# Kernel tuning notes

Measured on AMD Instinct MI355X. Metric: run time of the kernel, lower is better.

The kernel has to match this reference:

```python
import jax, jax.numpy as jnp
import numpy as np

EPS = 1e-5

def conv2d(x, w, pad):
    # x: [B,C,H,W], w: [O,I,kh,kw]
    return jax.lax.conv_general_dilated(x, w, window_strides=(1, 1),
                                        padding=[(pad, pad), (pad, pad)],
                                        dimension_numbers=('NCHW', 'OIHW', 'NCHW'))

def bn(x, g, b, m, v):
    # inference-mode BatchNorm2d
    scale = g / jnp.sqrt(v + EPS)
    return x * scale[None, :, None, None] + (b - m * scale)[None, :, None, None]

def setup_inputs() -> dict:
    key = jax.random.key(0)
    ks = jax.random.split(key, 12)
    B, C, H, W = 4, 256, 300, 300
    HC, NC, NREG = 64, 3, 8
    inp = {
        'bev_features': jax.random.normal(ks[0], (B, C, H, W), jnp.float32),
        'w_shared': jax.random.normal(ks[1], (HC, C, 3, 3), jnp.float32) * 0.02,
        'g_shared': jax.random.uniform(ks[2], (HC,), jnp.float32, 0.5, 1.5),
        'b_shared': jnp.zeros((HC,), jnp.float32),
        'm_shared': jnp.zeros((HC,), jnp.float32),
        'v_shared': jnp.ones((HC,), jnp.float32),
        'w_hm1': jax.random.normal(ks[3], (HC, HC, 3, 3), jnp.float32) * 0.05,
        'g_hm1': jax.random.uniform(ks[4], (HC,), jnp.float32, 0.5, 1.5),
        'b_hm1': jnp.zeros((HC,), jnp.float32),
        'm_hm1': jnp.zeros((HC,), jnp.float32),
        'v_hm1': jnp.ones((HC,), jnp.float32),
        'w_hm2': jax.random.normal(ks[5], (NC, HC, 1, 1), jnp.float32) * 0.05,
        'b_hm2': jnp.full((NC,), -2.19, jnp.float32),  # focal-loss prior init
        'w_reg1': jax.random.normal(ks[6], (HC, HC, 3, 3), jnp.float32) * 0.05,
        'g_reg1': jax.random.uniform(ks[7], (HC,), jnp.float32, 0.5, 1.5),
        'b_reg1': jnp.zeros((HC,), jnp.float32),
        'm_reg1': jnp.zeros((HC,), jnp.float32),
        'v_reg1': jnp.ones((HC,), jnp.float32),
        'w_reg2': jax.random.normal(ks[8], (NREG, HC, 1, 1), jnp.float32) * 0.05,
        'b_reg2': jnp.zeros((NREG,), jnp.float32),
    }
    return inp

def reference(bev_features, w_shared, g_shared, b_shared, m_shared, v_shared,
              w_hm1, g_hm1, b_hm1, m_hm1, v_hm1, w_hm2, b_hm2,
              w_reg1, g_reg1, b_reg1, m_reg1, v_reg1, w_reg2, b_reg2):
    # shared trunk: conv3x3 -> BN -> ReLU
    shared = jax.nn.relu(bn(conv2d(bev_features, w_shared, 1), g_shared, b_shared, m_shared, v_shared))
    # heatmap head: conv3x3 -> BN -> ReLU -> conv1x1(+bias)
    hm = jax.nn.relu(bn(conv2d(shared, w_hm1, 1), g_hm1, b_hm1, m_hm1, v_hm1))
    heatmap = conv2d(hm, w_hm2, 0) + b_hm2[None, :, None, None]
    rg = jax.nn.relu(bn(conv2d(shared, w_reg1, 1), g_reg1, b_reg1, m_reg1, v_reg1))
    box_reg = conv2d(rg, w_reg2, 0) + b_reg2[None, :, None, None]
    return heatmap, box_reg
```

## Files before the change

kernel.cpp:

```cpp
#include <hip/hip_runtime.h>


typedef __attribute__((ext_vector_type(8))) short bf16x8;
typedef __attribute__((ext_vector_type(4))) float f32x4;

#define WIMG 300
#define HW 90000

__device__ __forceinline__ unsigned short f2bf(float f) {
    unsigned u = __float_as_uint(f);
    u += 0x7fff + ((u >> 16) & 1);
    return (unsigned short)(u >> 16);
}

__device__ __forceinline__ void gload16(const unsigned short* g, unsigned short* l) {
    __builtin_amdgcn_global_load_lds(
        (const __attribute__((address_space(1))) void*)g,
        (__attribute__((address_space(3))) void*)l, 16, 0, 0);
}

__global__ __launch_bounds__(256) void nchw2nhwc_bf16_k(
    const float* __restrict__ in_all,
    unsigned short* __restrict__ out_all)
{
    __shared__ unsigned short lds[32][132];
    const int p0 = blockIdx.x * 128;
    const int c0 = blockIdx.y * 32;
    const int b = blockIdx.z;
    const float* in = in_all + (size_t)b * 256 * HW;
    unsigned short* out = out_all + (size_t)b * HW * 256;
    const int t = threadIdx.x;

#pragma unroll
    for (int i = 0; i < 4; ++i) {
        int task = i * 256 + t;
        int c = task >> 5;
        int p4 = (task & 31) * 4;
        const float* src = in + (size_t)(c0 + c) * HW + p0 + p4;
        float4 v;
        if (p0 + p4 + 3 < HW) {
            v = *(const float4*)src;
        } else {
            v.x = (p0 + p4 + 0 < HW) ? src[0] : 0.f;
            v.y = (p0 + p4 + 1 < HW) ? src[1] : 0.f;
            v.z = (p0 + p4 + 2 < HW) ? src[2] : 0.f;
            v.w = (p0 + p4 + 3 < HW) ? src[3] : 0.f;
        }
        uint2 pk;
        pk.x = (unsigned)f2bf(v.x) | ((unsigned)f2bf(v.y) << 16);
        pk.y = (unsigned)f2bf(v.z) | ((unsigned)f2bf(v.w) << 16);
        *(uint2*)&lds[c][p4] = pk;
    }
    __syncthreads();

    const int ct = t & 7;
    const int pt = t >> 3;
    uint2 r[4];
#pragma unroll
    for (int j = 0; j < 4; ++j)
        r[j] = *(const uint2*)&lds[ct * 4 + j][pt * 4];
#pragma unroll
    for (int i = 0; i < 4; ++i) {
        unsigned e0 = (((i < 2) ? r[0].x : r[0].y) >> ((i & 1) * 16)) & 0xffffu;
        unsigned e1 = (((i < 2) ? r[1].x : r[1].y) >> ((i & 1) * 16)) & 0xffffu;
        unsigned e2 = (((i < 2) ? r[2].x : r[2].y) >> ((i & 1) * 16)) & 0xffffu;
        unsigned e3 = (((i < 2) ? r[3].x : r[3].y) >> ((i & 1) * 16)) & 0xffffu;
        uint2 o;
        o.x = e0 | (e1 << 16);
        o.y = e2 | (e3 << 16);
        int px = p0 + pt * 4 + i;
        if (px < HW)
            *(uint2*)&out[(size_t)px * 256 + c0 + ct * 4] = o;
    }
}

__global__ __launch_bounds__(256) void pack_w_k(
    const float* __restrict__ w, unsigned short* __restrict__ apack, int CIN)
{
    const int KSUB = CIN / 32;
    const int tot = 9 * KSUB * 4 * 64 * 8;
    int idx = blockIdx.x * 256 + threadIdx.x;
    if (idx >= tot) return;
    int j = idx & 7;
    int lane = (idx >> 3) & 63;
    int rest = idx >> 9;
    int mt = rest & 3;
    int rest2 = rest >> 2;
    int ks = rest2 % KSUB;
    int tap = rest2 / KSUB;
    int oc = mt * 16 + (lane & 15);
    int ic = ks * 32 + (lane >> 4) * 8 + j;
    apack[idx] = f2bf(w[((size_t)oc * CIN + ic) * 9 + tap]);
}

template <int CIN, int NOUT>
__global__ __launch_bounds__(256, 3) void conv3_mfma_k(
    const unsigned short* __restrict__ in_all,
    const uint4* __restrict__ apack,
    const float* __restrict__ gg, const float* __restrict__ bb,
    const float* __restrict__ mm, const float* __restrict__ vv,
    const float* __restrict__ w2, const float* __restrict__ b2,
    unsigned short* __restrict__ out_nhwc_all,
    float* __restrict__ out_f32_all,
    const unsigned short* __restrict__ zp)
{
    constexpr int KSUB = CIN / 32;
    constexpr int TASKS = 396 * 4;
    __shared__ uint4 lds4[2][1600];

    const int wave = threadIdx.x >> 6;
    const int lane = threadIdx.x & 63;
    const int n16 = lane & 15;
    const int quad = lane >> 4;
    const int x0 = blockIdx.x * 64;
    const int y0 = blockIdx.y * 4;
    const int y = y0 + wave;
    const int b = blockIdx.z;
    const unsigned short* inb = in_all + (size_t)b * HW * CIN;

    const unsigned short* sp[7];
#pragma unroll
    for (int i = 0; i < 7; ++i) {
        int task = i * 256 + wave * 64 + lane;
        int s = task & 3;
        int px = task >> 2;
        int r = px / 66;
        int c = px - r * 66;
        int ys = y0 - 1 + r;
        int xs = x0 - 1 + c;
        bool ok = (task < TASKS) && ((unsigned)ys < (unsigned)WIMG)
                                 && ((unsigned)xs < (unsigned)WIMG);
        sp[i] = ok ? (inb + ((size_t)ys * WIMG + xs) * CIN + s * 8) : zp;
    }

    f32x4 acc[4][4];
#pragma unroll
    for (int mt = 0; mt < 4; ++mt)
#pragma unroll
        for (int nt = 0; nt < 4; ++nt)
            acc[mt][nt] = (f32x4){0.f, 0.f, 0.f, 0.f};

    union U16 { uint4 u; bf16x8 h; };

    auto stage = [&](int buf, int ks) {
#pragma unroll
        for (int i = 0; i < 7; ++i) {
            int base = i * 256 + wave * 64;
            if (base < TASKS)
                gload16(sp[i] + ks * 32, (unsigned short*)&lds4[buf][base]);
        }
    };

    stage(0, 0);
    asm volatile("s_waitcnt vmcnt(0)" ::: "memory");
    __syncthreads();

    int cur = 0;
#pragma unroll 1
    for (int ks = 0; ks < KSUB; ++ks) {
        if (ks + 1 < KSUB)
            stage(cur ^ 1, ks + 1);
        const unsigned short* lp = (const unsigned short*)lds4[cur];
#pragma unroll
        for (int tap = 0; tap < 9; ++tap) {
            const int dy = tap / 3 - 1, dx = tap % 3 - 1;
            const int rbase = (wave + dy + 1) * 66 + dx + 1;
            U16 bf[4], a[4];
#pragma unroll
            for (int nt = 0; nt < 4; ++nt)
                bf[nt].u = *(const uint4*)(lp + (size_t)(rbase + nt * 16 + n16) * 32 + quad * 8);
#pragma unroll
            for (int mt = 0; mt < 4; ++mt)
                a[mt].u = apack[(size_t)(((tap * KSUB + ks) * 4 + mt) * 64) + lane];
#pragma unroll
            for (int mt = 0; mt < 4; ++mt)
#pragma unroll
                for (int nt = 0; nt < 4; ++nt)
                    acc[mt][nt] = __builtin_amdgcn_mfma_f32_16x16x32_bf16(
                        a[mt].h, bf[nt].h, acc[mt][nt], 0, 0, 0);
        }
        asm volatile("s_waitcnt vmcnt(0)" ::: "memory");
        __syncthreads();
        cur ^= 1;
    }

    float scl[4][4], sft[4][4];
#pragma unroll
    for (int mt = 0; mt < 4; ++mt)
#pragma unroll
        for (int j = 0; j < 4; ++j) {
            int c = mt * 16 + quad * 4 + j;
            float s = gg[c] / sqrtf(vv[c] + 1e-5f);
            scl[mt][j] = s;
            sft[mt][j] = bb[c] - mm[c] * s;
        }

    if (NOUT == 0) {
        unsigned short* outb = out_nhwc_all + (size_t)b * HW * 64;
#pragma unroll
        for (int nt = 0; nt < 4; ++nt) {
            int xg = x0 + nt * 16 + n16;
            if (xg < WIMG) {
                unsigned short* op = outb + ((size_t)y * WIMG + xg) * 64 + quad * 4;
#pragma unroll
                for (int mt = 0; mt < 4; ++mt) {
                    union { unsigned short s[4]; uint2 u; } pk;
#pragma unroll
                    for (int j = 0; j < 4; ++j) {
                        float t = acc[mt][nt][j] * scl[mt][j] + sft[mt][j];
                        pk.s[j] = f2bf(t > 0.f ? t : 0.f);
                    }
                    *(uint2*)(op + mt * 16) = pk.u;
                }
            }
        }
    } else {
#pragma unroll
        for (int mt = 0; mt < 4; ++mt)
#pragma unroll
            for (int nt = 0; nt < 4; ++nt)
#pragma unroll
                for (int j = 0; j < 4; ++j) {
                    float t = acc[mt][nt][j] * scl[mt][j] + sft[mt][j];
                    acc[mt][nt][j] = t > 0.f ? t : 0.f;
                }
        float* outb = out_f32_all + (size_t)b * NOUT * HW;
#pragma unroll
        for (int no = 0; no < NOUT; ++no) {
            float wv[4][4];
#pragma unroll
            for (int mt = 0; mt < 4; ++mt)
#pragma unroll
                for (int j = 0; j < 4; ++j)
                    wv[mt][j] = w2[no * 64 + mt * 16 + quad * 4 + j];
#pragma unroll
            for (int nt = 0; nt < 4; ++nt) {
                float s = 0.f;
#pragma unroll
                for (int mt = 0; mt < 4; ++mt)
#pragma unroll
                    for (int j = 0; j < 4; ++j)
                        s += acc[mt][nt][j] * wv[mt][j];
                s += __shfl_xor(s, 16);
                s += __shfl_xor(s, 32);
                int xg = x0 + nt * 16 + n16;
                if (((no & 3) == quad) && xg < WIMG)
                    outb[(size_t)no * HW + (size_t)y * WIMG + xg] = s + b2[no];
            }
        }
    }
}

extern "C" void kernel_launch(void* const* d_in, const int* in_sizes, int n_in,
                              void* d_out, int out_size, void* d_ws, size_t ws_size,
                              hipStream_t stream) {
    const float* bev    = (const float*)d_in[0];
    const float* w_sh   = (const float*)d_in[1];
    const float* g_sh   = (const float*)d_in[2];
    const float* b_sh   = (const float*)d_in[3];
    const float* m_sh   = (const float*)d_in[4];
    const float* v_sh   = (const float*)d_in[5];
    const float* w_hm1  = (const float*)d_in[6];
    const float* g_hm1  = (const float*)d_in[7];
    const float* b_hm1  = (const float*)d_in[8];
    const float* m_hm1  = (const float*)d_in[9];
    const float* v_hm1  = (const float*)d_in[10];
    const float* w_hm2  = (const float*)d_in[11];
    const float* b_hm2  = (const float*)d_in[12];
    const float* w_reg1 = (const float*)d_in[13];
    const float* g_reg1 = (const float*)d_in[14];
    const float* b_reg1 = (const float*)d_in[15];
    const float* m_reg1 = (const float*)d_in[16];
    const float* v_reg1 = (const float*)d_in[17];
    const float* w_reg2 = (const float*)d_in[18];
    const float* b_reg2 = (const float*)d_in[19];

    char* ws = (char*)d_ws;
    unsigned short* inbuf     = (unsigned short*)(ws);
    unsigned short* sharedbuf = (unsigned short*)(ws + 184320000);
    unsigned short* apk1      = (unsigned short*)(ws + 230400000);
    unsigned short* apkh      = (unsigned short*)(ws + 230694912);
    unsigned short* apkr      = (unsigned short*)(ws + 230768640);
    unsigned short* zp        = (unsigned short*)(ws + 230842368);

    float* heatmap = (float*)d_out;
    float* box_reg = heatmap + (size_t)4 * 3 * HW;

    hipMemsetAsync(zp, 0, 4096, stream);

    pack_w_k<<<dim3(576), 256, 0, stream>>>(w_sh, apk1, 256);
    pack_w_k<<<dim3(144), 256, 0, stream>>>(w_hm1, apkh, 64);
    pack_w_k<<<dim3(144), 256, 0, stream>>>(w_reg1, apkr, 64);

    nchw2nhwc_bf16_k<<<dim3(704, 8, 4), 256, 0, stream>>>(bev, inbuf);

    const dim3 cgrid(5, 75, 4);
    conv3_mfma_k<256, 0><<<cgrid, 256, 0, stream>>>(
        inbuf, (const uint4*)apk1, g_sh, b_sh, m_sh, v_sh,
        nullptr, nullptr, sharedbuf, nullptr, zp);
    conv3_mfma_k<64, 3><<<cgrid, 256, 0, stream>>>(
        sharedbuf, (const uint4*)apkh, g_hm1, b_hm1, m_hm1, v_hm1,
        w_hm2, b_hm2, nullptr, heatmap, zp);
    conv3_mfma_k<64, 8><<<cgrid, 256, 0, stream>>>(
        sharedbuf, (const uint4*)apkr, g_reg1, b_reg1, m_reg1, v_reg1,
        w_reg2, b_reg2, nullptr, box_reg, zp);
}
```

Baseline: 817.1 us.

## Fuse heatmap and regression head convs into one kernel, add XCD block swizzle

The two 64-channel head convolutions become one kernel that stages the shared feature tile into LDS once and runs MFMAs for both weight sets, instead of two launches that each reread the shared buffer. The trunk and head kernels also remap block IDs so neighbouring tiles land on the same XCD, which should improve L2 reuse of halo rows. The fused kernel doubles the accumulator registers, so its occupancy bound drops from 3 to 2 blocks per CU.

```diff
diff --git a/kernel.cpp b/kernel.cpp
--- a/kernel.cpp
+++ b/kernel.cpp
@@ -6,6 +6,7 @@
 
 #define WIMG 300
 #define HW 90000
+#define NWG 1500
 
 __device__ __forceinline__ unsigned short f2bf(float f) {
     unsigned u = __float_as_uint(f);
@@ -17,6 +18,18 @@
     __builtin_amdgcn_global_load_lds(
         (const __attribute__((address_space(1))) void*)g,
         (__attribute__((address_space(3))) void*)l, 16, 0, 0);
+}
+
+__device__ __forceinline__ void swz_block(int& bx, int& by, int& bz) {
+    const int orig = blockIdx.x + 5 * (blockIdx.y + 75 * blockIdx.z);
+    const int q = NWG / 8, r = NWG % 8;
+    const int xcd = orig & 7, i = orig >> 3;
+    const int wg = (xcd < r) ? xcd * (q + 1) + i
+                             : r * (q + 1) + (xcd - r) * q + i;
+    bx = wg % 5;
+    const int rest = wg / 5;
+    by = rest % 75;
+    bz = rest / 75;
 }
 
 __global__ __launch_bounds__(256) void nchw2nhwc_bf16_k(
@@ -93,32 +106,13 @@
     apack[idx] = f2bf(w[((size_t)oc * CIN + ic) * 9 + tap]);
 }
 
-template <int CIN, int NOUT>
-__global__ __launch_bounds__(256, 3) void conv3_mfma_k(
-    const unsigned short* __restrict__ in_all,
-    const uint4* __restrict__ apack,
-    const float* __restrict__ gg, const float* __restrict__ bb,
-    const float* __restrict__ mm, const float* __restrict__ vv,
-    const float* __restrict__ w2, const float* __restrict__ b2,
-    unsigned short* __restrict__ out_nhwc_all,
-    float* __restrict__ out_f32_all,
-    const unsigned short* __restrict__ zp)
-{
-    constexpr int KSUB = CIN / 32;
-    constexpr int TASKS = 396 * 4;
-    __shared__ uint4 lds4[2][1600];
-
-    const int wave = threadIdx.x >> 6;
-    const int lane = threadIdx.x & 63;
-    const int n16 = lane & 15;
-    const int quad = lane >> 4;
-    const int x0 = blockIdx.x * 64;
-    const int y0 = blockIdx.y * 4;
-    const int y = y0 + wave;
-    const int b = blockIdx.z;
-    const unsigned short* inb = in_all + (size_t)b * HW * CIN;
-
-    const unsigned short* sp[7];
+#define TASKS (396 * 4)
+
+template <int CIN>
+__device__ __forceinline__ void make_sp(const unsigned short* inb,
+                                        const unsigned short* zp,
+                                        int x0, int y0, int wave, int lane,
+                                        const unsigned short* (&sp)[7]) {
 #pragma unroll
     for (int i = 0; i < 7; ++i) {
         int task = i * 256 + wave * 64 + lane;
@@ -132,6 +126,42 @@
                                  && ((unsigned)xs < (unsigned)WIMG);
         sp[i] = ok ? (inb + ((size_t)ys * WIMG + xs) * CIN + s * 8) : zp;
     }
+}
+
+__device__ __forceinline__ void stage_ks(const unsigned short* const (&sp)[7],
+                                         uint4* dst, int wave, int ks) {
+#pragma unroll
+    for (int i = 0; i < 7; ++i) {
+        int base = i * 256 + wave * 64;
+        if (base < TASKS)
+            gload16(sp[i] + ks * 32, (unsigned short*)&dst[base]);
+    }
+}
+
+__global__ __launch_bounds__(256, 3) void conv3_trunk_k(
+    const unsigned short* __restrict__ in_all,
+    const uint4* __restrict__ apack,
+    const float* __restrict__ gg, const float* __restrict__ bb,
+    const float* __restrict__ mm, const float* __restrict__ vv,
+    unsigned short* __restrict__ out_nhwc_all,
+    const unsigned short* __restrict__ zp)
+{
+    constexpr int CIN = 256, KSUB = 8;
+    __shared__ uint4 lds4[2][1600];
+
+    const int wave = threadIdx.x >> 6;
+    const int lane = threadIdx.x & 63;
+    const int n16 = lane & 15;
+    const int quad = lane >> 4;
+    int bx, by, b;
+    swz_block(bx, by, b);
+    const int x0 = bx * 64;
+    const int y0 = by * 4;
+    const int y = y0 + wave;
+    const unsigned short* inb = in_all + (size_t)b * HW * CIN;
+
+    const unsigned short* sp[7];
+    make_sp<CIN>(inb, zp, x0, y0, wave, lane, sp);
 
     f32x4 acc[4][4];
 #pragma unroll
@@ -142,16 +172,7 @@
 
     union U16 { uint4 u; bf16x8 h; };
 
-    auto stage = [&](int buf, int ks) {
-#pragma unroll
-        for (int i = 0; i < 7; ++i) {
-            int base = i * 256 + wave * 64;
-            if (base < TASKS)
-                gload16(sp[i] + ks * 32, (unsigned short*)&lds4[buf][base]);
-        }
-    };
-
-    stage(0, 0);
+    stage_ks(sp, lds4[0], wave, 0);
     asm volatile("s_waitcnt vmcnt(0)" ::: "memory");
     __syncthreads();
 
@@ -159,7 +180,7 @@
 #pragma unroll 1
     for (int ks = 0; ks < KSUB; ++ks) {
         if (ks + 1 < KSUB)
-            stage(cur ^ 1, ks + 1);
+            stage_ks(sp, lds4[cur ^ 1], wave, ks + 1);
         const unsigned short* lp = (const unsigned short*)lds4[cur];
 #pragma unroll
         for (int tap = 0; tap < 9; ++tap) {
@@ -195,26 +216,119 @@
             sft[mt][j] = bb[c] - mm[c] * s;
         }
 
-    if (NOUT == 0) {
-        unsigned short* outb = out_nhwc_all + (size_t)b * HW * 64;
+    unsigned short* outb = out_nhwc_all + (size_t)b * HW * 64;
+#pragma unroll
+    for (int nt = 0; nt < 4; ++nt) {
+        int xg = x0 + nt * 16 + n16;
+        if (xg < WIMG) {
+            unsigned short* op = outb + ((size_t)y * WIMG + xg) * 64 + quad * 4;
+#pragma unroll
+            for (int mt = 0; mt < 4; ++mt) {
+                union { unsigned short s[4]; uint2 u; } pk;
+#pragma unroll
+                for (int j = 0; j < 4; ++j) {
+                    float t = acc[mt][nt][j] * scl[mt][j] + sft[mt][j];
+                    pk.s[j] = f2bf(t > 0.f ? t : 0.f);
+                }
+                *(uint2*)(op + mt * 16) = pk.u;
+            }
+        }
+    }
+}
+
+__global__ __launch_bounds__(256, 2) void conv3_dualhead_k(
+    const unsigned short* __restrict__ in_all,
+    const uint4* __restrict__ apack_h,
+    const uint4* __restrict__ apack_r,
+    const float* __restrict__ g_h, const float* __restrict__ b_h,
+    const float* __restrict__ m_h, const float* __restrict__ v_h,
+    const float* __restrict__ g_r, const float* __restrict__ b_r,
+    const float* __restrict__ m_r, const float* __restrict__ v_r,
+    const float* __restrict__ w2_h, const float* __restrict__ b2_h,
+    const float* __restrict__ w2_r, const float* __restrict__ b2_r,
+    float* __restrict__ out_h_all,
+    float* __restrict__ out_r_all,
+    const unsigned short* __restrict__ zp)
+{
+    constexpr int CIN = 64, KSUB = 2;
+    __shared__ uint4 lds4[2][1600];
+
+    const int wave = threadIdx.x >> 6;
+    const int lane = threadIdx.x & 63;
+    const int n16 = lane & 15;
+    const int quad = lane >> 4;
+    int bx, by, b;
+    swz_block(bx, by, b);
+    const int x0 = bx * 64;
+    const int y0 = by * 4;
+    const int y = y0 + wave;
+    const unsigned short* inb = in_all + (size_t)b * HW * CIN;
+
+    const unsigned short* sp[7];
+    make_sp<CIN>(inb, zp, x0, y0, wave, lane, sp);
+
+    f32x4 acch[4][4], accr[4][4];
+#pragma unroll
+    for (int mt = 0; mt < 4; ++mt)
 #pragma unroll
         for (int nt = 0; nt < 4; ++nt) {
-            int xg = x0 + nt * 16 + n16;
-            if (xg < WIMG) {
-                unsigned short* op = outb + ((size_t)y * WIMG + xg) * 64 + quad * 4;
-#pragma unroll
-                for (int mt = 0; mt < 4; ++mt) {
-                    union { unsigned short s[4]; uint2 u; } pk;
-#pragma unroll
-                    for (int j = 0; j < 4; ++j) {
-                        float t = acc[mt][nt][j] * scl[mt][j] + sft[mt][j];
-                        pk.s[j] = f2bf(t > 0.f ? t : 0.f);
-                    }
-                    *(uint2*)(op + mt * 16) = pk.u;
+            acch[mt][nt] = (f32x4){0.f, 0.f, 0.f, 0.f};
+            accr[mt][nt] = (f32x4){0.f, 0.f, 0.f, 0.f};
+        }
+
+    union U16 { uint4 u; bf16x8 h; };
+
+    stage_ks(sp, lds4[0], wave, 0);
+    asm volatile("s_waitcnt vmcnt(0)" ::: "memory");
+    __syncthreads();
+
+    int cur = 0;
+#pragma unroll 1
+    for (int ks = 0; ks < KSUB; ++ks) {
+        if (ks + 1 < KSUB)
+            stage_ks(sp, lds4[cur ^ 1], wave, ks + 1);
+        const unsigned short* lp = (const unsigned short*)lds4[cur];
+#pragma unroll
+        for (int tap = 0; tap < 9; ++tap) {
+            const int dy = tap / 3 - 1, dx = tap % 3 - 1;
+            const int rbase = (wave + dy + 1) * 66 + dx + 1;
+            U16 bf[4];
+#pragma unroll
+            for (int nt = 0; nt < 4; ++nt)
+                bf[nt].u = *(const uint4*)(lp + (size_t)(rbase + nt * 16 + n16) * 32 + quad * 8);
+#pragma unroll
+            for (int mt = 0; mt < 4; ++mt) {
+                U16 ah, ar;
+                size_t ai = (size_t)(((tap * KSUB + ks) * 4 + mt) * 64) + lane;
+                ah.u = apack_h[ai];
+                ar.u = apack_r[ai];
+#pragma unroll
+                for (int nt = 0; nt < 4; ++nt) {
+                    acch[mt][nt] = __builtin_amdgcn_mfma_f32_16x16x32_bf16(
+                        ah.h, bf[nt].h, acch[mt][nt], 0, 0, 0);
+                    accr[mt][nt] = __builtin_amdgcn_mfma_f32_16x16x32_bf16(
+                        ar.h, bf[nt].h, accr[mt][nt], 0, 0, 0);
                 }
             }
         }
-    } else {
+        asm volatile("s_waitcnt vmcnt(0)" ::: "memory");
+        __syncthreads();
+        cur ^= 1;
+    }
+
+    auto epi = [&](f32x4 (&acc)[4][4], const float* gg, const float* bb,
+                   const float* mm, const float* vv, const float* w2,
+                   const float* b2, int NOUT, float* outb) {
+        float scl[4][4], sft[4][4];
+#pragma unroll
+        for (int mt = 0; mt < 4; ++mt)
+#pragma unroll
+            for (int j = 0; j < 4; ++j) {
+                int c = mt * 16 + quad * 4 + j;
+                float s = gg[c] / sqrtf(vv[c] + 1e-5f);
+                scl[mt][j] = s;
+                sft[mt][j] = bb[c] - mm[c] * s;
+            }
 #pragma unroll
         for (int mt = 0; mt < 4; ++mt)
 #pragma unroll
@@ -224,8 +338,6 @@
                     float t = acc[mt][nt][j] * scl[mt][j] + sft[mt][j];
                     acc[mt][nt][j] = t > 0.f ? t : 0.f;
                 }
-        float* outb = out_f32_all + (size_t)b * NOUT * HW;
-#pragma unroll
         for (int no = 0; no < NOUT; ++no) {
             float wv[4][4];
 #pragma unroll
@@ -248,7 +360,10 @@
                     outb[(size_t)no * HW + (size_t)y * WIMG + xg] = s + b2[no];
             }
         }
-    }
+    };
+
+    epi(acch, g_h, b_h, m_h, v_h, w2_h, b2_h, 3, out_h_all + (size_t)b * 3 * HW);
+    epi(accr, g_r, b_r, m_r, v_r, w2_r, b2_r, 8, out_r_all + (size_t)b * 8 * HW);
 }
 
 extern "C" void kernel_launch(void* const* d_in, const int* in_sizes, int n_in,
@@ -295,13 +410,12 @@
     nchw2nhwc_bf16_k<<<dim3(704, 8, 4), 256, 0, stream>>>(bev, inbuf);
 
     const dim3 cgrid(5, 75, 4);
-    conv3_mfma_k<256, 0><<<cgrid, 256, 0, stream>>>(
-        inbuf, (const uint4*)apk1, g_sh, b_sh, m_sh, v_sh,
-        nullptr, nullptr, sharedbuf, nullptr, zp);
-    conv3_mfma_k<64, 3><<<cgrid, 256, 0, stream>>>(
-        sharedbuf, (const uint4*)apkh, g_hm1, b_hm1, m_hm1, v_hm1,
-        w_hm2, b_hm2, nullptr, heatmap, zp);
-    conv3_mfma_k<64, 8><<<cgrid, 256, 0, stream>>>(
-        sharedbuf, (const uint4*)apkr, g_reg1, b_reg1, m_reg1, v_reg1,
-        w_reg2, b_reg2, nullptr, box_reg, zp);
-}
+    conv3_trunk_k<<<cgrid, 256, 0, stream>>>(
+        inbuf, (const uint4*)apk1, g_sh, b_sh, m_sh, v_sh, sharedbuf, zp);
+    conv3_dualhead_k<<<cgrid, 256, 0, stream>>>(
+        sharedbuf, (const uint4*)apkh, (const uint4*)apkr,
+        g_hm1, b_hm1, m_hm1, v_hm1,
+        g_reg1, b_reg1, m_reg1, v_reg1,
+        w_hm2, b_hm2, w_reg2, b_reg2,
+        heatmap, box_reg, zp);
+}
```

After: 816.1 us. Within noise of the previous version (-0.1%).
